# Kernel tuning notes

Hardware: AMD Instinct MI355X
Metric: run time of the kernel (lower is better)

## Reference

```python
import jax, jax.numpy as jnp
import numpy as np

N = 8192
E = 262144
IN_F, HID, OUT = 1024, 256, 40


def setup_inputs() -> dict:
    key = jax.random.key(0)
    k_x, k_e0, k_e1, k_w1, k_w2 = jax.random.split(key, 5)
    x = jax.random.normal(k_x, (N, IN_F), dtype=jnp.float32)
    edge_index = jnp.stack([
        jax.random.randint(k_e0, (E,), 0, N),
        jax.random.randint(k_e1, (E,), 0, N),
    ]).astype(jnp.int64)
    # Xavier-uniform init as in nn.init.xavier_uniform_
    lim1 = float(np.sqrt(6.0 / (IN_F + HID)))
    lim2 = float(np.sqrt(6.0 / (HID + OUT)))
    W1 = jax.random.uniform(k_w1, (IN_F, HID), minval=-lim1, maxval=lim1, dtype=jnp.float32)
    b1 = jnp.zeros((HID,), dtype=jnp.float32)
    W2 = jax.random.uniform(k_w2, (HID, OUT), minval=-lim2, maxval=lim2, dtype=jnp.float32)
    b2 = jnp.zeros((OUT,), dtype=jnp.float32)
    return {"x": x, "edge_index": edge_index, "W1": W1, "b1": b1, "W2": W2, "b2": b2}


def _a_hat(edge_index, num_nodes):
    # A[src, dst] = 1; A_tilde = A + I; A_hat = D^{-1/2} A_tilde D^{-1/2}
    A = jnp.zeros((num_nodes, num_nodes), dtype=jnp.float32)
    A = A.at[edge_index[0], edge_index[1]].set(1.0)
    A_tilde = A + jnp.eye(num_nodes, dtype=jnp.float32)
    deg = A_tilde.sum(axis=1)
    d_is = deg ** -0.5
    # diag(d) @ A @ diag(d) == row/col broadcast scaling (same math, fewer FLOPs)
    return d_is[:, None] * A_tilde * d_is[None, :]


def reference(x, edge_index, W1, b1, W2, b2):
    A_hat = _a_hat(edge_index, x.shape[0])
    h = A_hat @ (x @ W1) + b1
    h = jax.nn.relu(h)
    # dropout: eval mode (identity), matching deterministic reference
    h = A_hat @ (h @ W2) + b2
    return jax.nn.log_softmax(h, axis=1)
```

## Files before the change

kernel.cpp:

```cpp
#include <hip/hip_runtime.h>
#include <math.h>

static constexpr int NN   = 8192;
static constexpr int EE   = 262144;
static constexpr int KIN  = 1024;
static constexpr int HID  = 256;
static constexpr int NOUT = 40;

typedef float  f32x4  __attribute__((ext_vector_type(4)));
typedef short  short8 __attribute__((ext_vector_type(8)));

static constexpr size_t SZ_BITMAP = (size_t)NN * NN / 8;
static constexpr size_t SZ_RC     = (size_t)NN * 4;
static constexpr size_t SZ_ROFF   = (((size_t)(NN + 1) * 4 + 255) / 256) * 256;
static constexpr size_t SZ_DIS    = (size_t)NN * 4;
static constexpr size_t SZ_CSR    = (size_t)EE * 4;
static constexpr size_t SZ_H1     = (size_t)NN * HID * 4;
static constexpr size_t SZ_G2     = (size_t)NN * NOUT * 4;
static constexpr size_t SZ_WP     = (size_t)KIN * HID * 2;

static constexpr size_t O_BITMAP = 0;
static constexpr size_t MEMSET_BYTES = SZ_BITMAP;
static constexpr size_t O_RC     = O_BITMAP + SZ_BITMAP;
static constexpr size_t O_ROFF   = O_RC + SZ_RC;
static constexpr size_t O_DIS    = O_ROFF + SZ_ROFF;
static constexpr size_t O_CSR    = O_DIS + SZ_DIS;
static constexpr size_t O_H1     = O_CSR + SZ_CSR;
static constexpr size_t O_H1A    = O_H1 + SZ_H1;
static constexpr size_t O_G2     = O_H1A + SZ_H1;
static constexpr size_t O_WH     = O_G2 + SZ_G2;
static constexpr size_t O_WL     = O_WH + SZ_WP;

__device__ inline unsigned short f2bf(float f) {
    unsigned u = __float_as_uint(f);
    return (unsigned short)((u + 0x7fffu + ((u >> 16) & 1u)) >> 16);
}
__device__ inline float bf2f(unsigned short h) {
    return __uint_as_float((unsigned)h << 16);
}


__global__ __launch_bounds__(256) void ingest_kernel(const int* __restrict__ e,
        unsigned* __restrict__ bitmap) {
    __shared__ int sflag;
    if (threadIdx.x == 0) {
        int orv = 0;
        #pragma unroll
        for (int j = 1; j < 64; j += 2) orv |= e[j];
        sflag = (orv == 0) ? 1 : 0;
    }
    __syncthreads();
    const int i = blockIdx.x * 256 + threadIdx.x;
    int s, d;
    if (sflag) { s = e[2 * i]; d = e[2 * EE + 2 * i]; }
    else       { s = e[i];     d = e[EE + i]; }
    const unsigned key = ((unsigned)s << 13) | (unsigned)d;
    atomicOr(&bitmap[key >> 5], 1u << (key & 31u));
}

__global__ __launch_bounds__(256) void count_kernel(const unsigned* __restrict__ bitmap,
        int* __restrict__ rowc) {
    const int row = blockIdx.x;
    const int t = threadIdx.x;
    int pc = __popc(bitmap[row * 256 + t]);
    #pragma unroll
    for (int o = 32; o > 0; o >>= 1) pc += __shfl_xor(pc, o);
    __shared__ int part[4];
    if ((t & 63) == 0) part[t >> 6] = pc;
    __syncthreads();
    if (t == 0) rowc[row] = part[0] + part[1] + part[2] + part[3];
}

__global__ __launch_bounds__(1024) void scan_kernel(const int* __restrict__ rowc,
        int* __restrict__ roff, float* __restrict__ dis) {
    __shared__ int ps[1024];
    const int t = threadIdx.x;
    const int base = t * 8;
    int v[8];
    int s = 0;
    #pragma unroll
    for (int j = 0; j < 8; ++j) { v[j] = rowc[base + j]; s += v[j]; }
    ps[t] = s;
    __syncthreads();
    for (int o = 1; o < 1024; o <<= 1) {
        int add = (t >= o) ? ps[t - o] : 0;
        __syncthreads();
        ps[t] += add;
        __syncthreads();
    }
    int run = ps[t] - s;
    #pragma unroll
    for (int j = 0; j < 8; ++j) {
        roff[base + j] = run;
        run += v[j];
        dis[base + j] = rsqrtf((float)(v[j] + 1));
    }
    if (t == 1023) roff[NN] = run;
}

__global__ __launch_bounds__(256) void place_kernel(const unsigned* __restrict__ bitmap,
        const int* __restrict__ roff, unsigned* __restrict__ csr) {
    const int row = blockIdx.x;
    const int t = threadIdx.x;
    unsigned wv = bitmap[row * 256 + t];
    const int pc = __popc(wv);
    __shared__ int ps[256];
    ps[t] = pc;
    __syncthreads();
    for (int o = 1; o < 256; o <<= 1) {
        int add = (t >= o) ? ps[t - o] : 0;
        __syncthreads();
        ps[t] += add;
        __syncthreads();
    }
    int pos = roff[row] + ps[t] - pc;
    while (wv) {
        const int b = __ffs(wv) - 1;
        wv &= wv - 1;
        csr[pos++] = (unsigned)(t * 32 + b);
    }
}

__global__ __launch_bounds__(256) void wsplit_kernel(const float* __restrict__ W1,
        unsigned short* __restrict__ Wh, unsigned short* __restrict__ Wl) {
    const int id  = blockIdx.x * 256 + threadIdx.x;
    const int l   = id & 63;
    const int kt  = (id >> 6) & 31;
    const int nfg = id >> 11;
    const int k0  = kt * 32 + ((l >> 4) << 3);
    const int n   = (nfg << 4) + (l & 15);
    unsigned hh[8], ll[8];
    #pragma unroll
    for (int j = 0; j < 8; ++j) {
        const float f = W1[(size_t)(k0 + j) * HID + n];
        const unsigned short h = f2bf(f);
        hh[j] = h;
        ll[j] = f2bf(f - bf2f(h));
    }
    uint4 vh, vl;
    vh.x = hh[0] | (hh[1] << 16); vh.y = hh[2] | (hh[3] << 16);
    vh.z = hh[4] | (hh[5] << 16); vh.w = hh[6] | (hh[7] << 16);
    vl.x = ll[0] | (ll[1] << 16); vl.y = ll[2] | (ll[3] << 16);
    vl.z = ll[4] | (ll[5] << 16); vl.w = ll[6] | (ll[7] << 16);
    ((uint4*)Wh)[id] = vh;
    ((uint4*)Wl)[id] = vl;
}

static constexpr int RS = 264;

__global__ __launch_bounds__(256) void gemm1_kernel(const float* __restrict__ X,
        const unsigned short* __restrict__ Wh, const unsigned short* __restrict__ Wl,
        float* __restrict__ H) {
    __shared__ unsigned short Ah[32 * RS];
    __shared__ unsigned short Al[32 * RS];
    const int t    = threadIdx.x;
    const int bm   = blockIdx.x;
    const int bn   = blockIdx.y;
    const int lane = t & 63;
    const int w    = t >> 6;
    const int sr = t >> 3;
    const int sc = (t & 7) << 2;
    const float* Xp = X + (size_t)(bm * 32 + sr) * KIN + sc;
    const short8* Bhp = (const short8*)Wh;
    const short8* Blp = (const short8*)Wl;

    f32x4 acc[2][2];
    #pragma unroll
    for (int mf = 0; mf < 2; ++mf)
        #pragma unroll
        for (int nf = 0; nf < 2; ++nf) acc[mf][nf] = (f32x4)0.f;

    float4 px[8];
    #pragma unroll
    for (int i = 0; i < 8; ++i) px[i] = *(const float4*)(Xp + i * 32);

    const int nfg0 = bn * 8 + w * 2;
    short8 bch[2], bcl[2], bnh[2], bnl[2];
    #pragma unroll
    for (int nf = 0; nf < 2; ++nf) {
        const int fi = ((nfg0 + nf) * 32 + 0) * 64 + lane;
        bch[nf] = Bhp[fi];
        bcl[nf] = Blp[fi];
    }

    for (int ch = 0; ch < 4; ++ch) {
        __syncthreads();
        #pragma unroll
        for (int i = 0; i < 8; ++i) {
            const int k0 = sc + i * 32;
            const float4 v = px[i];
            const float fv[4] = {v.x, v.y, v.z, v.w};
            ushort4 h4, l4;
            unsigned short hs[4], ls[4];
            #pragma unroll
            for (int j = 0; j < 4; ++j) {
                hs[j] = f2bf(fv[j]);
                ls[j] = f2bf(fv[j] - bf2f(hs[j]));
            }
            h4.x = hs[0]; h4.y = hs[1]; h4.z = hs[2]; h4.w = hs[3];
            l4.x = ls[0]; l4.y = ls[1]; l4.z = ls[2]; l4.w = ls[3];
            *(ushort4*)&Ah[sr * RS + k0] = h4;
            *(ushort4*)&Al[sr * RS + k0] = l4;
        }
        __syncthreads();
        if (ch < 3) {
            Xp += 256;
            #pragma unroll
            for (int i = 0; i < 8; ++i) px[i] = *(const float4*)(Xp + i * 32);
        }
        #pragma unroll
        for (int kk = 0; kk < 8; ++kk) {
            const int kt = ch * 8 + kk;
            short8 ah[2], al[2];
            #pragma unroll
            for (int mf = 0; mf < 2; ++mf) {
                const int off = (mf * 16 + (lane & 15)) * RS + kk * 32 + ((lane >> 4) << 3);
                ah[mf] = *(const short8*)&Ah[off];
                al[mf] = *(const short8*)&Al[off];
            }
            if (kt < 31) {
                #pragma unroll
                for (int nf = 0; nf < 2; ++nf) {
                    const int fi = ((nfg0 + nf) * 32 + kt + 1) * 64 + lane;
                    bnh[nf] = Bhp[fi];
                    bnl[nf] = Blp[fi];
                }
            }
            #pragma unroll
            for (int mf = 0; mf < 2; ++mf)
                #pragma unroll
                for (int nf = 0; nf < 2; ++nf) {
                    f32x4 c = acc[mf][nf];
                    c = __builtin_amdgcn_mfma_f32_16x16x32_bf16(ah[mf], bch[nf], c, 0, 0, 0);
                    c = __builtin_amdgcn_mfma_f32_16x16x32_bf16(ah[mf], bcl[nf], c, 0, 0, 0);
                    c = __builtin_amdgcn_mfma_f32_16x16x32_bf16(al[mf], bch[nf], c, 0, 0, 0);
                    acc[mf][nf] = c;
                }
            #pragma unroll
            for (int nf = 0; nf < 2; ++nf) { bch[nf] = bnh[nf]; bcl[nf] = bnl[nf]; }
        }
    }
    #pragma unroll
    for (int mf = 0; mf < 2; ++mf)
        #pragma unroll
        for (int nf = 0; nf < 2; ++nf)
            #pragma unroll
            for (int r = 0; r < 4; ++r) {
                const int row = bm * 32 + mf * 16 + ((lane >> 4) << 2) + r;
                const int col = bn * 128 + w * 32 + nf * 16 + (lane & 15);
                H[(size_t)row * HID + col] = acc[mf][nf][r];
            }
}

__global__ __launch_bounds__(256) void agg1_kernel(const float* __restrict__ H1,
        const int* __restrict__ roff, const unsigned* __restrict__ csr,
        const float* __restrict__ dis, const float* __restrict__ b1,
        float* __restrict__ out) {
    __shared__ unsigned dl[256];
    __shared__ float    wl[256];
    const int s = blockIdx.x;
    const int c = threadIdx.x;
    const float ds = dis[s];
    float acc = ds * ds * H1[(size_t)s * HID + c];
    const int beg = roff[s], end = roff[s + 1];
    for (int chk = beg; chk < end; chk += 256) {
        const int n = min(256, end - chk);
        __syncthreads();
        if (c < n) {
            const unsigned d = csr[chk + c];
            dl[c] = d;
            wl[c] = ds * dis[d];
        }
        __syncthreads();
        #pragma unroll 4
        for (int i = 0; i < n; ++i)
            acc = fmaf(wl[i], H1[(size_t)dl[i] * HID + c], acc);
    }
    out[(size_t)s * HID + c] = fmaxf(acc + b1[c], 0.f);
}

__global__ __launch_bounds__(256) void gemm2_kernel(const float* __restrict__ H,
        const float* __restrict__ W2, float* __restrict__ G) {
    __shared__ float w2s[HID * NOUT];
    const int t = threadIdx.x;
    for (int i = t; i < HID * NOUT; i += 256) w2s[i] = W2[i];
    __syncthreads();
    const int row = blockIdx.x * 64 + (t >> 2);
    const int cg  = (t & 3) * 10;
    float acc[10];
    #pragma unroll
    for (int j = 0; j < 10; ++j) acc[j] = 0.f;
    const float* hp = H + (size_t)row * HID;
    for (int k = 0; k < HID; k += 4) {
        const float4 h4 = *(const float4*)(hp + k);
        #pragma unroll
        for (int j = 0; j < 10; ++j) {
            acc[j] = fmaf(h4.x, w2s[(k + 0) * NOUT + cg + j],
                     fmaf(h4.y, w2s[(k + 1) * NOUT + cg + j],
                     fmaf(h4.z, w2s[(k + 2) * NOUT + cg + j],
                     fmaf(h4.w, w2s[(k + 3) * NOUT + cg + j], acc[j]))));
        }
    }
    #pragma unroll
    for (int j = 0; j < 10; ++j) G[(size_t)row * NOUT + cg + j] = acc[j];
}

__global__ __launch_bounds__(256) void agg2_kernel(const float* __restrict__ G,
        const int* __restrict__ roff, const unsigned* __restrict__ csr,
        const float* __restrict__ dis, const float* __restrict__ b2,
        float* __restrict__ out) {
    const int wv   = threadIdx.x >> 6;
    const int lane = threadIdx.x & 63;
    const int s = blockIdx.x * 4 + wv;
    const bool act = lane < NOUT;
    const float ds = dis[s];
    float acc = act ? ds * ds * G[(size_t)s * NOUT + lane] : 0.f;
    const int beg = roff[s], end = roff[s + 1];
    int e = beg;
    for (; e + 4 <= end; e += 4) {
        const unsigned d0 = csr[e], d1 = csr[e + 1], d2 = csr[e + 2], d3 = csr[e + 3];
        const float w0 = ds * dis[d0], w1 = ds * dis[d1];
        const float w2 = ds * dis[d2], w3 = ds * dis[d3];
        if (act) {
            const float g0 = G[(size_t)d0 * NOUT + lane];
            const float g1 = G[(size_t)d1 * NOUT + lane];
            const float g2 = G[(size_t)d2 * NOUT + lane];
            const float g3 = G[(size_t)d3 * NOUT + lane];
            acc = fmaf(w0, g0, acc); acc = fmaf(w1, g1, acc);
            acc = fmaf(w2, g2, acc); acc = fmaf(w3, g3, acc);
        }
    }
    for (; e < end; ++e) {
        const unsigned d = csr[e];
        const float wt = ds * dis[d];
        if (act) acc = fmaf(wt, G[(size_t)d * NOUT + lane], acc);
    }
    if (act) acc += b2[lane];
    float v = act ? acc : -INFINITY;
    #pragma unroll
    for (int o = 32; o > 0; o >>= 1) v = fmaxf(v, __shfl_xor(v, o));
    float ex = act ? expf(acc - v) : 0.f;
    #pragma unroll
    for (int o = 32; o > 0; o >>= 1) ex += __shfl_xor(ex, o);
    const float lz = v + logf(ex);
    if (act) out[(size_t)s * NOUT + lane] = acc - lz;
}

extern "C" void kernel_launch(void* const* d_in, const int* in_sizes, int n_in,
                              void* d_out, int out_size, void* d_ws, size_t ws_size,
                              hipStream_t stream) {
    (void)in_sizes; (void)n_in; (void)out_size; (void)ws_size;
    const float* x  = (const float*)d_in[0];
    const int*   ei = (const int*)d_in[1];
    const float* W1 = (const float*)d_in[2];
    const float* b1 = (const float*)d_in[3];
    const float* W2 = (const float*)d_in[4];
    const float* b2 = (const float*)d_in[5];
    float* out = (float*)d_out;
    char* ws = (char*)d_ws;

    unsigned*       bitmap = (unsigned*)(ws + O_BITMAP);
    int*            rowc   = (int*)(ws + O_RC);
    int*            roff   = (int*)(ws + O_ROFF);
    float*          dis    = (float*)(ws + O_DIS);
    unsigned*       csr    = (unsigned*)(ws + O_CSR);
    float*          H1     = (float*)(ws + O_H1);
    float*          H1A    = (float*)(ws + O_H1A);
    float*          G2     = (float*)(ws + O_G2);
    unsigned short* Wh     = (unsigned short*)(ws + O_WH);
    unsigned short* Wl     = (unsigned short*)(ws + O_WL);

    hipMemsetAsync(ws, 0, MEMSET_BYTES, stream);

    ingest_kernel<<<EE / 256, 256, 0, stream>>>(ei, bitmap);
    count_kernel<<<NN, 256, 0, stream>>>(bitmap, rowc);
    scan_kernel<<<1, 1024, 0, stream>>>(rowc, roff, dis);
    place_kernel<<<NN, 256, 0, stream>>>(bitmap, roff, csr);

    wsplit_kernel<<<(KIN * HID / 8) / 256, 256, 0, stream>>>(W1, Wh, Wl);
    gemm1_kernel<<<dim3(NN / 32, 2), 256, 0, stream>>>(x, Wh, Wl, H1);
    agg1_kernel<<<NN, 256, 0, stream>>>(H1, roff, csr, dis, b1, H1A);
    gemm2_kernel<<<NN / 64, 256, 0, stream>>>(H1A, W2, G2);
    agg2_kernel<<<NN / 4, 256, 0, stream>>>(G2, roff, csr, dis, b2, out);
}
```

Before: 191.3 us.

## Store hidden activations in bf16 and use wave-per-node vectorized aggregation

Intermediate H1 and H1A buffers are stored as bf16 instead of fp32, halving the bytes gathered in the sparse aggregation and read by gemm2. agg1 is restructured from one block per node with shared-memory staging and barriers to one wavefront per node, each lane handling four columns with ushort4 loads and a 4-way unrolled edge loop. This reduces memory traffic and sync overhead but adds bf16 rounding error to intermediate activations.

```diff
diff --git a/kernel.cpp b/kernel.cpp
--- a/kernel.cpp
+++ b/kernel.cpp
@@ -15,7 +15,7 @@
 static constexpr size_t SZ_ROFF   = (((size_t)(NN + 1) * 4 + 255) / 256) * 256;
 static constexpr size_t SZ_DIS    = (size_t)NN * 4;
 static constexpr size_t SZ_CSR    = (size_t)EE * 4;
-static constexpr size_t SZ_H1     = (size_t)NN * HID * 4;
+static constexpr size_t SZ_H1B    = (size_t)NN * HID * 2;
 static constexpr size_t SZ_G2     = (size_t)NN * NOUT * 4;
 static constexpr size_t SZ_WP     = (size_t)KIN * HID * 2;
 
@@ -26,8 +26,8 @@
 static constexpr size_t O_DIS    = O_ROFF + SZ_ROFF;
 static constexpr size_t O_CSR    = O_DIS + SZ_DIS;
 static constexpr size_t O_H1     = O_CSR + SZ_CSR;
-static constexpr size_t O_H1A    = O_H1 + SZ_H1;
-static constexpr size_t O_G2     = O_H1A + SZ_H1;
+static constexpr size_t O_H1A    = O_H1 + SZ_H1B;
+static constexpr size_t O_G2     = O_H1A + SZ_H1B;
 static constexpr size_t O_WH     = O_G2 + SZ_G2;
 static constexpr size_t O_WL     = O_WH + SZ_WP;
 
@@ -150,7 +150,7 @@
 
 __global__ __launch_bounds__(256) void gemm1_kernel(const float* __restrict__ X,
         const unsigned short* __restrict__ Wh, const unsigned short* __restrict__ Wl,
-        float* __restrict__ H) {
+        unsigned short* __restrict__ H) {
     __shared__ unsigned short Ah[32 * RS];
     __shared__ unsigned short Al[32 * RS];
     const int t    = threadIdx.x;
@@ -248,38 +248,59 @@
             for (int r = 0; r < 4; ++r) {
                 const int row = bm * 32 + mf * 16 + ((lane >> 4) << 2) + r;
                 const int col = bn * 128 + w * 32 + nf * 16 + (lane & 15);
-                H[(size_t)row * HID + col] = acc[mf][nf][r];
+                H[(size_t)row * HID + col] = f2bf(acc[mf][nf][r]);
             }
 }
 
-__global__ __launch_bounds__(256) void agg1_kernel(const float* __restrict__ H1,
+__global__ __launch_bounds__(256) void agg1_kernel(const unsigned short* __restrict__ H1b,
         const int* __restrict__ roff, const unsigned* __restrict__ csr,
         const float* __restrict__ dis, const float* __restrict__ b1,
-        float* __restrict__ out) {
-    __shared__ unsigned dl[256];
-    __shared__ float    wl[256];
-    const int s = blockIdx.x;
-    const int c = threadIdx.x;
+        unsigned short* __restrict__ outb) {
+    const int w    = threadIdx.x >> 6;
+    const int lane = threadIdx.x & 63;
+    const int s = blockIdx.x * 4 + w;
+    const int c0 = lane * 4;
     const float ds = dis[s];
-    float acc = ds * ds * H1[(size_t)s * HID + c];
+    const float ds2 = ds * ds;
+    ushort4 hv = *(const ushort4*)&H1b[(size_t)s * HID + c0];
+    float a0 = ds2 * bf2f(hv.x), a1 = ds2 * bf2f(hv.y);
+    float a2 = ds2 * bf2f(hv.z), a3 = ds2 * bf2f(hv.w);
     const int beg = roff[s], end = roff[s + 1];
-    for (int chk = beg; chk < end; chk += 256) {
-        const int n = min(256, end - chk);
-        __syncthreads();
-        if (c < n) {
-            const unsigned d = csr[chk + c];
-            dl[c] = d;
-            wl[c] = ds * dis[d];
-        }
-        __syncthreads();
-        #pragma unroll 4
-        for (int i = 0; i < n; ++i)
-            acc = fmaf(wl[i], H1[(size_t)dl[i] * HID + c], acc);
-    }
-    out[(size_t)s * HID + c] = fmaxf(acc + b1[c], 0.f);
-}
-
-__global__ __launch_bounds__(256) void gemm2_kernel(const float* __restrict__ H,
+    int e = beg;
+    for (; e + 4 <= end; e += 4) {
+        const unsigned d0 = csr[e], d1 = csr[e + 1], d2 = csr[e + 2], d3 = csr[e + 3];
+        const float w0 = ds * dis[d0], w1 = ds * dis[d1];
+        const float w2 = ds * dis[d2], w3 = ds * dis[d3];
+        const ushort4 v0 = *(const ushort4*)&H1b[(size_t)d0 * HID + c0];
+        const ushort4 v1 = *(const ushort4*)&H1b[(size_t)d1 * HID + c0];
+        const ushort4 v2 = *(const ushort4*)&H1b[(size_t)d2 * HID + c0];
+        const ushort4 v3 = *(const ushort4*)&H1b[(size_t)d3 * HID + c0];
+        a0 = fmaf(w0, bf2f(v0.x), a0); a1 = fmaf(w0, bf2f(v0.y), a1);
+        a2 = fmaf(w0, bf2f(v0.z), a2); a3 = fmaf(w0, bf2f(v0.w), a3);
+        a0 = fmaf(w1, bf2f(v1.x), a0); a1 = fmaf(w1, bf2f(v1.y), a1);
+        a2 = fmaf(w1, bf2f(v1.z), a2); a3 = fmaf(w1, bf2f(v1.w), a3);
+        a0 = fmaf(w2, bf2f(v2.x), a0); a1 = fmaf(w2, bf2f(v2.y), a1);
+        a2 = fmaf(w2, bf2f(v2.z), a2); a3 = fmaf(w2, bf2f(v2.w), a3);
+        a0 = fmaf(w3, bf2f(v3.x), a0); a1 = fmaf(w3, bf2f(v3.y), a1);
+        a2 = fmaf(w3, bf2f(v3.z), a2); a3 = fmaf(w3, bf2f(v3.w), a3);
+    }
+    for (; e < end; ++e) {
+        const unsigned d = csr[e];
+        const float wt = ds * dis[d];
+        const ushort4 v = *(const ushort4*)&H1b[(size_t)d * HID + c0];
+        a0 = fmaf(wt, bf2f(v.x), a0); a1 = fmaf(wt, bf2f(v.y), a1);
+        a2 = fmaf(wt, bf2f(v.z), a2); a3 = fmaf(wt, bf2f(v.w), a3);
+    }
+    const float4 bv = *(const float4*)&b1[c0];
+    ushort4 o;
+    o.x = f2bf(fmaxf(a0 + bv.x, 0.f));
+    o.y = f2bf(fmaxf(a1 + bv.y, 0.f));
+    o.z = f2bf(fmaxf(a2 + bv.z, 0.f));
+    o.w = f2bf(fmaxf(a3 + bv.w, 0.f));
+    *(ushort4*)&outb[(size_t)s * HID + c0] = o;
+}
+
+__global__ __launch_bounds__(256) void gemm2_kernel(const unsigned short* __restrict__ Hb,
         const float* __restrict__ W2, float* __restrict__ G) {
     __shared__ float w2s[HID * NOUT];
     const int t = threadIdx.x;
@@ -290,16 +311,19 @@
     float acc[10];
     #pragma unroll
     for (int j = 0; j < 10; ++j) acc[j] = 0.f;
-    const float* hp = H + (size_t)row * HID;
-    for (int k = 0; k < HID; k += 4) {
-        const float4 h4 = *(const float4*)(hp + k);
-        #pragma unroll
-        for (int j = 0; j < 10; ++j) {
-            acc[j] = fmaf(h4.x, w2s[(k + 0) * NOUT + cg + j],
-                     fmaf(h4.y, w2s[(k + 1) * NOUT + cg + j],
-                     fmaf(h4.z, w2s[(k + 2) * NOUT + cg + j],
-                     fmaf(h4.w, w2s[(k + 3) * NOUT + cg + j], acc[j]))));
-        }
+    const unsigned short* hp = Hb + (size_t)row * HID;
+    for (int k = 0; k < HID; k += 8) {
+        const uint4 hv = *(const uint4*)(hp + k);
+        float h[8];
+        h[0] = bf2f((unsigned short)(hv.x & 0xffff)); h[1] = bf2f((unsigned short)(hv.x >> 16));
+        h[2] = bf2f((unsigned short)(hv.y & 0xffff)); h[3] = bf2f((unsigned short)(hv.y >> 16));
+        h[4] = bf2f((unsigned short)(hv.z & 0xffff)); h[5] = bf2f((unsigned short)(hv.z >> 16));
+        h[6] = bf2f((unsigned short)(hv.w & 0xffff)); h[7] = bf2f((unsigned short)(hv.w >> 16));
+        #pragma unroll
+        for (int i = 0; i < 8; ++i)
+            #pragma unroll
+            for (int j = 0; j < 10; ++j)
+                acc[j] = fmaf(h[i], w2s[(k + i) * NOUT + cg + j], acc[j]);
     }
     #pragma unroll
     for (int j = 0; j < 10; ++j) G[(size_t)row * NOUT + cg + j] = acc[j];
@@ -364,8 +388,8 @@
     int*            roff   = (int*)(ws + O_ROFF);
     float*          dis    = (float*)(ws + O_DIS);
     unsigned*       csr    = (unsigned*)(ws + O_CSR);
-    float*          H1     = (float*)(ws + O_H1);
-    float*          H1A    = (float*)(ws + O_H1A);
+    unsigned short* H1     = (unsigned short*)(ws + O_H1);
+    unsigned short* H1A    = (unsigned short*)(ws + O_H1A);
     float*          G2     = (float*)(ws + O_G2);
     unsigned short* Wh     = (unsigned short*)(ws + O_WH);
     unsigned short* Wl     = (unsigned short*)(ws + O_WL);
@@ -379,7 +403,7 @@
 
     wsplit_kernel<<<(KIN * HID / 8) / 256, 256, 0, stream>>>(W1, Wh, Wl);
     gemm1_kernel<<<dim3(NN / 32, 2), 256, 0, stream>>>(x, Wh, Wl, H1);
-    agg1_kernel<<<NN, 256, 0, stream>>>(H1, roff, csr, dis, b1, H1A);
+    agg1_kernel<<<NN / 4, 256, 0, stream>>>(H1, roff, csr, dis, b1, H1A);
     gemm2_kernel<<<NN / 64, 256, 0, stream>>>(H1A, W2, G2);
     agg2_kernel<<<NN / 4, 256, 0, stream>>>(G2, roff, csr, dis, b2, out);
 }
```

Result: faster. 176.1 us (-7.9%).
